# Kernel tuning notes

Measured on AMD Instinct MI355X. Metric: run time of the kernel, lower is better.

Reference implementation:

```python
import jax, jax.numpy as jnp
import numpy as np

SAMPLING_RATE = 16000.0
SINE_AMP = 0.1
NOISE_STD = 0.003
HARMONIC_NUM = 8  # dim = 9


def setup_inputs() -> dict:
    key = jax.random.key(0)
    k1, k2, k3, k4, k5, k6 = jax.random.split(key, 6)
    B, T, D = 16, 65536, HARMONIC_NUM + 1
    f0 = jax.random.uniform(k1, (B, T, 1), dtype=jnp.float32) * 400.0
    voiced = (jax.random.uniform(k2, (B, T, 1)) > 0.2).astype(jnp.float32)
    f0 = f0 * voiced
    # random initial phase per (batch, harmonic); first harmonic gets phase 0
    rand_init = jax.random.uniform(k3, (B, D), dtype=jnp.float32)
    rand_init = rand_init.at[:, 0].set(0.0)
    noise = jax.random.normal(k4, (B, T, D), dtype=jnp.float32)
    W = jax.random.normal(k5, (1, D), dtype=jnp.float32) * (1.0 / np.sqrt(D))
    b = jax.random.normal(k6, (1,), dtype=jnp.float32) * 0.01
    return {"f0": f0, "rand_init": rand_init, "noise": noise, "W": W, "b": b}


def reference(f0, rand_init, noise, W, b):
    # f0: [B, T, 1]; rand_init: [B, 9]; noise: [B, T, 9]; W: [1, 9]; b: [1]
    harmonics = jnp.arange(1, HARMONIC_NUM + 2, dtype=f0.dtype)  # [9]
    fn = f0 * harmonics                                          # [B, T, 9]
    rad = (fn / SAMPLING_RATE) % 1.0
    rad = rad.at[:, 0, :].add(rand_init)
    # phase-unwrap correction: subtract 1 wherever cumulative phase wrapped
    tmp = jnp.cumsum(rad, axis=1) % 1.0                          # [B, T, 9]
    diff = tmp[:, 1:, :] - tmp[:, :-1, :]                        # [B, T-1, 9]
    shift = jnp.concatenate(
        [jnp.zeros_like(rad[:, :1, :]), jnp.where(diff < 0, -1.0, 0.0)], axis=1
    )
    sines = jnp.sin(jnp.cumsum(rad + shift, axis=1) * (2.0 * jnp.pi)) * SINE_AMP
    uv = (f0 > 0.0).astype(f0.dtype)                             # [B, T, 1]
    noise_amp = uv * NOISE_STD + (1.0 - uv) * (SINE_AMP / 3.0)
    sine_waves = sines * uv + noise_amp * noise                  # [B, T, 9]
    sine_merge = jnp.tanh(sine_waves @ W.T + b)                  # [B, T, 1]
    return sine_merge
```

## Files before the change

kernel.cpp:

```cpp
#include <hip/hip_runtime.h>
#include <math.h>

#define B_N    16
#define T_LEN  65536
#define D_N    9
#define CHUNK  256
#define NCH    (T_LEN / CHUNK)

#define RCP_SR (1.0f / 16000.0f)

#define AS1C(p) ((const __attribute__((address_space(1))) void*)(p))
#define AS3(p)  ((__attribute__((address_space(3))) void*)(p))

__global__ __launch_bounds__(256) void k_chunksum(const float* __restrict__ f0,
                                                  float* __restrict__ csum) {
    int tid  = threadIdx.x;
    int lane = tid & 63;
    int wid  = tid >> 6;
    int chunk = blockIdx.x * 4 + wid;
    int b = chunk >> 8;
    int c = chunk & 255;
    int t = c * CHUNK + lane * 4;
    size_t bt = (size_t)b * T_LEN + t;

    const float4 fv = *reinterpret_cast<const float4*>(f0 + bt);
    double s = (double)(fv.x * RCP_SR) + (double)(fv.y * RCP_SR)
             + (double)(fv.z * RCP_SR) + (double)(fv.w * RCP_SR);

    #pragma unroll
    for (int off = 32; off >= 1; off >>= 1)
        s += __shfl_down(s, off, 64);

    if (lane == 0) {
        double fr = s - floor(s);
        csum[(size_t)b * NCH + c] = (float)fr;
    }
}

#define WAITV(n) asm volatile("s_waitcnt vmcnt(" #n ")" ::: "memory")

#define CONS(Q) do {                                                        \
    float4 v4 = ldsw[9 * lane + (Q)];                                       \
    dacc[(4*(Q)+0)/9] = fmaf(wreg[(4*(Q)+0)%9], v4.x, dacc[(4*(Q)+0)/9]);   \
    dacc[(4*(Q)+1)/9] = fmaf(wreg[(4*(Q)+1)%9], v4.y, dacc[(4*(Q)+1)/9]);   \
    dacc[(4*(Q)+2)/9] = fmaf(wreg[(4*(Q)+2)%9], v4.z, dacc[(4*(Q)+2)/9]);   \
    dacc[(4*(Q)+3)/9] = fmaf(wreg[(4*(Q)+3)%9], v4.w, dacc[(4*(Q)+3)/9]);   \
} while (0)

__global__ __launch_bounds__(256, 4) void k_main(const float* __restrict__ f0,
                                                 const float* __restrict__ noise,
                                                 const float* __restrict__ W,
                                                 const float* __restrict__ bias,
                                                 const float* __restrict__ rinit,
                                                 const float* __restrict__ csum,
                                                 float* __restrict__ out) {
    __shared__ float4 ldsbuf[4 * 576];
    int tid  = threadIdx.x;
    int lane = tid & 63;
    int wid  = tid >> 6;
    int chunk = blockIdx.x * 4 + wid;
    int b = chunk >> 8;
    int c = chunk & 255;
    int t = c * CHUNK + lane * 4;
    size_t bt = (size_t)b * T_LEN + t;

    const float4 fv  = *reinterpret_cast<const float4*>(f0 + bt);
    const float4 cs4 = *reinterpret_cast<const float4*>(csum + (size_t)b * NCH + lane * 4);

    int bu = __builtin_amdgcn_readfirstlane(b);
    const float* ri = rinit + bu * D_N;
    float wreg[D_N], rireg[D_N];
    #pragma unroll
    for (int h = 0; h < D_N; ++h) { wreg[h] = W[h]; rireg[h] = ri[h]; }
    float bb = bias[0];

    __builtin_amdgcn_sched_barrier(0);

    float4* ldsw = ldsbuf + wid * 576;
    const float* nbase = noise + ((size_t)b * T_LEN + (size_t)c * CHUNK) * D_N;
    #pragma unroll
    for (int q = 0; q < 9; ++q) {
        const float* g = nbase + (size_t)(lane + 64 * q) * 4;
        __builtin_amdgcn_global_load_lds(AS1C(g), AS3(ldsw + q * 64), 16, 0, 0);
    }
    __builtin_amdgcn_sched_barrier(0);

    float f[4] = {fv.x, fv.y, fv.z, fv.w};
    float s[4];
    float run = 0.0f;
    #pragma unroll
    for (int j = 0; j < 4; ++j) {
        run += f[j] * RCP_SR;
        s[j] = run;
    }
    float incl = run;
    #pragma unroll
    for (int off = 1; off < 64; off <<= 1) {
        float n = __shfl_up(incl, off, 64);
        if (lane >= off) incl += n;
    }

    int e0 = lane * 4;
    float pre = (e0 + 0 < c ? cs4.x : 0.0f)
              + (e0 + 1 < c ? cs4.y : 0.0f)
              + (e0 + 2 < c ? cs4.z : 0.0f)
              + (e0 + 3 < c ? cs4.w : 0.0f);
    #pragma unroll
    for (int off = 32; off >= 1; off >>= 1)
        pre += __shfl_xor(pre, off, 64);

    float base = __builtin_amdgcn_fractf(pre) + (incl - run);

    float fr[4], uvf[4], na[4];
    #pragma unroll
    for (int j = 0; j < 4; ++j) {
        fr[j] = __builtin_amdgcn_fractf(base + s[j]);
        bool uv = f[j] > 0.0f;
        uvf[j] = uv ? 0.1f : 0.0f;
        na[j]  = uv ? 0.003f : (float)(0.1 / 3.0);
    }

    float B[4] = {0.f, 0.f, 0.f, 0.f};
    #pragma unroll
    for (int h = 0; h < D_N; ++h) {
        const float hf = (float)(h + 1);
        const float wh = wreg[h];
        const float rih = rireg[h];
        #pragma unroll
        for (int j = 0; j < 4; ++j) {
            float x  = fmaf(fr[j], hf, rih);
            float xf = __builtin_amdgcn_fractf(x);
            float sn = __builtin_amdgcn_sinf(xf);
            B[j] = fmaf(sn, wh, B[j]);
        }
    }

    float dacc[4] = {0.f, 0.f, 0.f, 0.f};
    WAITV(8); CONS(0);
    WAITV(7); CONS(1);
    WAITV(6); CONS(2);
    WAITV(5); CONS(3);
    WAITV(4); CONS(4);
    WAITV(3); CONS(5);
    WAITV(2); CONS(6);
    WAITV(1); CONS(7);
    WAITV(0); CONS(8);

    float4 o;
    #pragma unroll
    for (int j = 0; j < 4; ++j) {
        float y = fmaf(na[j], dacc[j], fmaf(uvf[j], B[j], bb));
        float e = __expf(2.0f * y);
        float r = __builtin_amdgcn_rcpf(e + 1.0f);
        float th = 1.0f - 2.0f * r;
        (&o.x)[j] = th;
    }
    *reinterpret_cast<float4*>(out + bt) = o;
}

extern "C" void kernel_launch(void* const* d_in, const int* in_sizes, int n_in,
                              void* d_out, int out_size, void* d_ws, size_t ws_size,
                              hipStream_t stream) {
    const float* f0    = (const float*)d_in[0];
    const float* rinit = (const float*)d_in[1];
    const float* noise = (const float*)d_in[2];
    const float* W     = (const float*)d_in[3];
    const float* bias  = (const float*)d_in[4];
    float* out = (float*)d_out;

    float* csum = (float*)d_ws;

    k_chunksum<<<(B_N * NCH) / 4, 256, 0, stream>>>(f0, csum);
    k_main<<<(B_N * NCH) / 4, 256, 0, stream>>>(f0, noise, W, bias, rinit, csum, out);
}
```

Before: 17.90 us.

## Use fixed-point uint32 phase accumulation and double chunk size per wavefront

Phase is now accumulated as unsigned 32-bit fixed-point (f * 2^32/16000), so wraparound modulo 1 comes free from integer overflow. This removes the double-precision chunk sums, the floor call and the fract steps. Chunks grow from 256 to 512 samples, with 8 samples per lane and 18 LDS noise loads per wave, and blocks shrink to 128 threads. The trade-offs are quantisation of each step's phase and more registers and LDS per wave, which reduces occupancy.

```diff
diff --git a/kernel.cpp b/kernel.cpp
--- a/kernel.cpp
+++ b/kernel.cpp
@@ -4,68 +4,71 @@
 #define B_N    16
 #define T_LEN  65536
 #define D_N    9
-#define CHUNK  256
+#define CHUNK  512
 #define NCH    (T_LEN / CHUNK)
 
-#define RCP_SR (1.0f / 16000.0f)
+#define PHASE_SCALE 268435.456f
 
 #define AS1C(p) ((const __attribute__((address_space(1))) void*)(p))
 #define AS3(p)  ((__attribute__((address_space(3))) void*)(p))
 
+__device__ __forceinline__ unsigned int ph(float f) {
+    return (unsigned int)(f * PHASE_SCALE);
+}
+
 __global__ __launch_bounds__(256) void k_chunksum(const float* __restrict__ f0,
-                                                  float* __restrict__ csum) {
+                                                  unsigned int* __restrict__ csum) {
     int tid  = threadIdx.x;
     int lane = tid & 63;
     int wid  = tid >> 6;
     int chunk = blockIdx.x * 4 + wid;
-    int b = chunk >> 8;
-    int c = chunk & 255;
-    int t = c * CHUNK + lane * 4;
+    int b = chunk >> 7;
+    int c = chunk & 127;
+    int t = c * CHUNK + lane * 8;
     size_t bt = (size_t)b * T_LEN + t;
 
-    const float4 fv = *reinterpret_cast<const float4*>(f0 + bt);
-    double s = (double)(fv.x * RCP_SR) + (double)(fv.y * RCP_SR)
-             + (double)(fv.z * RCP_SR) + (double)(fv.w * RCP_SR);
+    const float4 a0 = *reinterpret_cast<const float4*>(f0 + bt);
+    const float4 a1 = *reinterpret_cast<const float4*>(f0 + bt + 4);
+    unsigned int s = ph(a0.x) + ph(a0.y) + ph(a0.z) + ph(a0.w)
+                   + ph(a1.x) + ph(a1.y) + ph(a1.z) + ph(a1.w);
 
     #pragma unroll
     for (int off = 32; off >= 1; off >>= 1)
         s += __shfl_down(s, off, 64);
 
-    if (lane == 0) {
-        double fr = s - floor(s);
-        csum[(size_t)b * NCH + c] = (float)fr;
-    }
+    if (lane == 0) csum[(size_t)b * NCH + c] = s;
 }
 
 #define WAITV(n) asm volatile("s_waitcnt vmcnt(" #n ")" ::: "memory")
 
 #define CONS(Q) do {                                                        \
-    float4 v4 = ldsw[9 * lane + (Q)];                                       \
+    float4 v4 = ldsw[18 * lane + (Q)];                                      \
     dacc[(4*(Q)+0)/9] = fmaf(wreg[(4*(Q)+0)%9], v4.x, dacc[(4*(Q)+0)/9]);   \
     dacc[(4*(Q)+1)/9] = fmaf(wreg[(4*(Q)+1)%9], v4.y, dacc[(4*(Q)+1)/9]);   \
     dacc[(4*(Q)+2)/9] = fmaf(wreg[(4*(Q)+2)%9], v4.z, dacc[(4*(Q)+2)/9]);   \
     dacc[(4*(Q)+3)/9] = fmaf(wreg[(4*(Q)+3)%9], v4.w, dacc[(4*(Q)+3)/9]);   \
 } while (0)
 
-__global__ __launch_bounds__(256, 4) void k_main(const float* __restrict__ f0,
+__global__ __launch_bounds__(128, 2) void k_main(const float* __restrict__ f0,
                                                  const float* __restrict__ noise,
                                                  const float* __restrict__ W,
                                                  const float* __restrict__ bias,
                                                  const float* __restrict__ rinit,
-                                                 const float* __restrict__ csum,
+                                                 const unsigned int* __restrict__ csum,
                                                  float* __restrict__ out) {
-    __shared__ float4 ldsbuf[4 * 576];
+    __shared__ float4 ldsbuf[2 * 1152];
     int tid  = threadIdx.x;
     int lane = tid & 63;
     int wid  = tid >> 6;
-    int chunk = blockIdx.x * 4 + wid;
-    int b = chunk >> 8;
-    int c = chunk & 255;
-    int t = c * CHUNK + lane * 4;
+    int chunk = blockIdx.x * 2 + wid;
+    int b = chunk >> 7;
+    int c = chunk & 127;
+    int t = c * CHUNK + lane * 8;
     size_t bt = (size_t)b * T_LEN + t;
 
-    const float4 fv  = *reinterpret_cast<const float4*>(f0 + bt);
-    const float4 cs4 = *reinterpret_cast<const float4*>(csum + (size_t)b * NCH + lane * 4);
+    const float4 a0 = *reinterpret_cast<const float4*>(f0 + bt);
+    const float4 a1 = *reinterpret_cast<const float4*>(f0 + bt + 4);
+    const uint2  cs2 = *reinterpret_cast<const uint2*>(csum + (size_t)b * NCH + lane * 2);
 
     int bu = __builtin_amdgcn_readfirstlane(b);
     const float* ri = rinit + bu * D_N;
@@ -76,58 +79,56 @@
 
     __builtin_amdgcn_sched_barrier(0);
 
-    float4* ldsw = ldsbuf + wid * 576;
+    float4* ldsw = ldsbuf + wid * 1152;
     const float* nbase = noise + ((size_t)b * T_LEN + (size_t)c * CHUNK) * D_N;
     #pragma unroll
-    for (int q = 0; q < 9; ++q) {
+    for (int q = 0; q < 18; ++q) {
         const float* g = nbase + (size_t)(lane + 64 * q) * 4;
         __builtin_amdgcn_global_load_lds(AS1C(g), AS3(ldsw + q * 64), 16, 0, 0);
     }
     __builtin_amdgcn_sched_barrier(0);
 
-    float f[4] = {fv.x, fv.y, fv.z, fv.w};
-    float s[4];
-    float run = 0.0f;
+    float f[8] = {a0.x, a0.y, a0.z, a0.w, a1.x, a1.y, a1.z, a1.w};
+    unsigned int s[8];
+    unsigned int run = 0u;
     #pragma unroll
-    for (int j = 0; j < 4; ++j) {
-        run += f[j] * RCP_SR;
+    for (int j = 0; j < 8; ++j) {
+        run += ph(f[j]);
         s[j] = run;
     }
-    float incl = run;
+    unsigned int incl = run;
     #pragma unroll
     for (int off = 1; off < 64; off <<= 1) {
-        float n = __shfl_up(incl, off, 64);
+        unsigned int n = __shfl_up(incl, off, 64);
         if (lane >= off) incl += n;
     }
 
-    int e0 = lane * 4;
-    float pre = (e0 + 0 < c ? cs4.x : 0.0f)
-              + (e0 + 1 < c ? cs4.y : 0.0f)
-              + (e0 + 2 < c ? cs4.z : 0.0f)
-              + (e0 + 3 < c ? cs4.w : 0.0f);
+    int e0 = lane * 2;
+    unsigned int pre = (e0 + 0 < c ? cs2.x : 0u)
+                     + (e0 + 1 < c ? cs2.y : 0u);
     #pragma unroll
     for (int off = 32; off >= 1; off >>= 1)
         pre += __shfl_xor(pre, off, 64);
 
-    float base = __builtin_amdgcn_fractf(pre) + (incl - run);
+    unsigned int base = pre + (incl - run);
 
-    float fr[4], uvf[4], na[4];
+    float fr[8], uvf[8], na[8];
     #pragma unroll
-    for (int j = 0; j < 4; ++j) {
-        fr[j] = __builtin_amdgcn_fractf(base + s[j]);
+    for (int j = 0; j < 8; ++j) {
+        fr[j] = (float)(base + s[j]) * (1.0f / 4294967296.0f);
         bool uv = f[j] > 0.0f;
         uvf[j] = uv ? 0.1f : 0.0f;
         na[j]  = uv ? 0.003f : (float)(0.1 / 3.0);
     }
 
-    float B[4] = {0.f, 0.f, 0.f, 0.f};
+    float B[8] = {0.f, 0.f, 0.f, 0.f, 0.f, 0.f, 0.f, 0.f};
     #pragma unroll
     for (int h = 0; h < D_N; ++h) {
         const float hf = (float)(h + 1);
         const float wh = wreg[h];
         const float rih = rireg[h];
         #pragma unroll
-        for (int j = 0; j < 4; ++j) {
+        for (int j = 0; j < 8; ++j) {
             float x  = fmaf(fr[j], hf, rih);
             float xf = __builtin_amdgcn_fractf(x);
             float sn = __builtin_amdgcn_sinf(xf);
@@ -135,27 +136,36 @@
         }
     }
 
-    float dacc[4] = {0.f, 0.f, 0.f, 0.f};
-    WAITV(8); CONS(0);
-    WAITV(7); CONS(1);
-    WAITV(6); CONS(2);
-    WAITV(5); CONS(3);
-    WAITV(4); CONS(4);
-    WAITV(3); CONS(5);
-    WAITV(2); CONS(6);
-    WAITV(1); CONS(7);
-    WAITV(0); CONS(8);
+    float dacc[8] = {0.f, 0.f, 0.f, 0.f, 0.f, 0.f, 0.f, 0.f};
+    WAITV(17); CONS(0);
+    WAITV(16); CONS(1);
+    WAITV(15); CONS(2);
+    WAITV(14); CONS(3);
+    WAITV(13); CONS(4);
+    WAITV(12); CONS(5);
+    WAITV(11); CONS(6);
+    WAITV(10); CONS(7);
+    WAITV(9);  CONS(8);
+    WAITV(8);  CONS(9);
+    WAITV(7);  CONS(10);
+    WAITV(6);  CONS(11);
+    WAITV(5);  CONS(12);
+    WAITV(4);  CONS(13);
+    WAITV(3);  CONS(14);
+    WAITV(2);  CONS(15);
+    WAITV(1);  CONS(16);
+    WAITV(0);  CONS(17);
 
-    float4 o;
+    float o[8];
     #pragma unroll
-    for (int j = 0; j < 4; ++j) {
+    for (int j = 0; j < 8; ++j) {
         float y = fmaf(na[j], dacc[j], fmaf(uvf[j], B[j], bb));
         float e = __expf(2.0f * y);
         float r = __builtin_amdgcn_rcpf(e + 1.0f);
-        float th = 1.0f - 2.0f * r;
-        (&o.x)[j] = th;
+        o[j] = 1.0f - 2.0f * r;
     }
-    *reinterpret_cast<float4*>(out + bt) = o;
+    *reinterpret_cast<float4*>(out + bt)     = make_float4(o[0], o[1], o[2], o[3]);
+    *reinterpret_cast<float4*>(out + bt + 4) = make_float4(o[4], o[5], o[6], o[7]);
 }
 
 extern "C" void kernel_launch(void* const* d_in, const int* in_sizes, int n_in,
@@ -168,8 +178,8 @@
     const float* bias  = (const float*)d_in[4];
     float* out = (float*)d_out;
 
-    float* csum = (float*)d_ws;
+    unsigned int* csum = (unsigned int*)d_ws;
 
     k_chunksum<<<(B_N * NCH) / 4, 256, 0, stream>>>(f0, csum);
-    k_main<<<(B_N * NCH) / 4, 256, 0, stream>>>(f0, noise, W, bias, rinit, csum, out);
+    k_main<<<(B_N * NCH) / 2, 128, 0, stream>>>(f0, noise, W, bias, rinit, csum, out);
 }
```

Measured after the change: 19.02 us. 1.06x slower.
